# Performance work log

Measured on AMD Instinct MI355X. Metric: run time of the kernel, lower is better.

Reference implementation:

```python
import jax, jax.numpy as jnp
import numpy as np
from jax import lax

B, T_DEC, T_ENC = 32, 400, 300
N_MEL, PRENET, ENC_D = 80, 256, 512
ATT_RNN, DEC_RNN, ATT_D = 512, 512, 128
LOC_F, LOC_K = 32, 31


def setup_inputs() -> dict:
    key = jax.random.key(0)
    ks = jax.random.split(key, 24)

    def w(k, shape):
        return jax.random.normal(k, shape, jnp.float32) / np.float32(np.sqrt(shape[-1]))

    inp = {
        "encoder_out": jax.random.normal(ks[0], (B, T_ENC, ENC_D), jnp.float32),
        "mels": jax.random.normal(ks[1], (B, T_DEC, N_MEL), jnp.float32),
        "lengths": jax.random.randint(ks[2], (B,), 1, T_ENC + 1).astype(jnp.int32),
        # prenet (3 layers, no bias)
        "W_p0": w(ks[3], (PRENET, N_MEL)),
        "W_p1": w(ks[4], (PRENET, PRENET)),
        "W_p2": w(ks[5], (PRENET, PRENET)),
        # attention GRUCell: input = prenet_dim + enc_dim = 768
        "W_ih_a": w(ks[6], (3 * ATT_RNN, PRENET + ENC_D)),
        "W_hh_a": w(ks[7], (3 * ATT_RNN, ATT_RNN)),
        "b_ih_a": jnp.zeros((3 * ATT_RNN,), jnp.float32),
        "b_hh_a": jnp.zeros((3 * ATT_RNN,), jnp.float32),
        # decoder GRUCell: input = attn_rnn + enc_dim = 1024 (what the code actually feeds)
        "W_ih_d": w(ks[8], (3 * DEC_RNN, ATT_RNN + ENC_D)),
        "W_hh_d": w(ks[9], (3 * DEC_RNN, DEC_RNN)),
        "b_ih_d": jnp.zeros((3 * DEC_RNN,), jnp.float32),
        "b_hh_d": jnp.zeros((3 * DEC_RNN,), jnp.float32),
        # location-sensitive attention
        "W_q": w(ks[10], (ATT_D, ATT_RNN)),
        "W_m": w(ks[11], (ATT_D, ENC_D)),
        "K_loc": w(ks[12], (LOC_F, 2, LOC_K)),
        "W_l": w(ks[13], (ATT_D, LOC_F)),
        "v": w(ks[14], (ATT_D,)),
        # output projection + gate
        "W_out": w(ks[15], (N_MEL, DEC_RNN + ENC_D)),
        "b_out": jnp.zeros((N_MEL,), jnp.float32),
        "W_g": w(ks[16], (1, DEC_RNN + ENC_D)),
        "b_g": jnp.zeros((1,), jnp.float32),
    }
    return inp


def _gru_cell(x, h, W_ih, W_hh, b_ih, b_hh):
    gi = x @ W_ih.T + b_ih
    gh = h @ W_hh.T + b_hh
    i_r, i_z, i_n = jnp.split(gi, 3, axis=-1)
    h_r, h_z, h_n = jnp.split(gh, 3, axis=-1)
    r = jax.nn.sigmoid(i_r + h_r)
    z = jax.nn.sigmoid(i_z + h_z)
    n = jnp.tanh(i_n + r * h_n)
    return (1.0 - z) * n + z * h


def _decoder_core(encoder_out, mels, lengths, W_p0, W_p1, W_p2,
                  W_ih_a, W_hh_a, b_ih_a, b_hh_a, W_ih_d, W_hh_d, b_ih_d, b_hh_d,
                  W_q, W_m, K_loc, W_l, v, W_out, b_out, W_g, b_g):
    Bb, T_enc, _ = encoder_out.shape
    T_dec = mels.shape[1]
    pmem = encoder_out @ W_m.T  # [B,T_enc,ATT_D], computed once
    enc_mask = jnp.arange(T_enc)[None, :] < lengths[:, None]  # [B,T_enc]
    # shifted teacher-forcing inputs: zero first frame, then mels[:, :-1]
    dec_inputs = jnp.concatenate(
        [jnp.zeros((Bb, 1, mels.shape[2]), mels.dtype), mels[:, :-1]], axis=1)
    drop_key = jax.random.key(42)
    pad = LOC_K // 2

    def prenet(x, t):
        for i, W in enumerate((W_p0, W_p1, W_p2)):
            x = jax.nn.relu(x @ W.T)
            k = jax.random.fold_in(drop_key, t * 3 + i)
            keep = jax.random.bernoulli(k, 0.5, x.shape)
            x = jnp.where(keep, x * 2.0, 0.0)  # inverted dropout p=0.5 (hardcoded training=True)
        return x

    def step(carry, xs):
        ah, dh, ctx, aw, aw_sum = carry
        frame, t = xs
        x = prenet(frame, t)
        ah = _gru_cell(jnp.concatenate([x, ctx], -1), ah, W_ih_a, W_hh_a, b_ih_a, b_hh_a)
        # location features from current + cumulative attention weights
        awc = jnp.stack([aw, aw_sum], axis=1)  # [B,2,T_enc]
        loc = lax.conv_general_dilated(awc, K_loc, (1,), [(pad, pad)],
                                       dimension_numbers=("NCH", "OIH", "NCH"))
        loc = jnp.swapaxes(loc, 1, 2) @ W_l.T  # [B,T_enc,ATT_D]
        e = jnp.tanh((ah @ W_q.T)[:, None, :] + pmem + loc) @ v  # [B,T_enc]
        e = jnp.where(enc_mask, e, -1e9)
        aw_new = jax.nn.softmax(e, axis=-1)
        ctx = jnp.einsum("bt,btd->bd", aw_new, encoder_out)
        aw_sum = aw_sum + aw_new
        dh = _gru_cell(jnp.concatenate([ah, ctx], -1), dh, W_ih_d, W_hh_d, b_ih_d, b_hh_d)
        dhc = jnp.concatenate([dh, ctx], -1)
        mel = dhc @ W_out.T + b_out  # [B,N_MEL]
        gate = (dhc @ W_g.T + b_g)[:, 0]  # [B]
        return (ah, dh, ctx, aw_new, aw_sum), (mel, gate, aw_new)

    f32 = encoder_out.dtype
    init = (jnp.zeros((Bb, ATT_RNN), f32), jnp.zeros((Bb, DEC_RNN), f32),
            jnp.zeros((Bb, ENC_D), f32), jnp.zeros((Bb, T_enc), f32),
            jnp.zeros((Bb, T_enc), f32))
    frames = jnp.swapaxes(dec_inputs, 0, 1)  # [T_dec,B,N_MEL]
    _, (mels_out, gates, aligns) = lax.scan(jax.checkpoint(step), init,
                                            (frames, jnp.arange(T_dec)))
    mel_outputs = jnp.transpose(mels_out, (1, 2, 0))  # [B,N_MEL,T_dec]
    gate_outputs = jnp.swapaxes(gates, 0, 1)          # [B,T_dec]
    alignments = jnp.swapaxes(aligns, 0, 1)           # [B,T_dec,T_enc]
    return mel_outputs, gate_outputs, alignments


def reference(encoder_out, mels, lengths, W_p0, W_p1, W_p2,
              W_ih_a, W_hh_a, b_ih_a, b_hh_a, W_ih_d, W_hh_d, b_ih_d, b_hh_d,
              W_q, W_m, K_loc, W_l, v, W_out, b_out, W_g, b_g):
    return _decoder_core(encoder_out, mels, lengths, W_p0, W_p1, W_p2,
                         W_ih_a, W_hh_a, b_ih_a, b_hh_a, W_ih_d, W_hh_d, b_ih_d, b_hh_d,
                         W_q, W_m, K_loc, W_l, v, W_out, b_out, W_g, b_g)
```

## Files before the change

### kernel.cpp

```cpp
#include <hip/hip_runtime.h>
#include <cstdint>


static constexpr int TDEC = 400, TENC = 300, NMEL = 80;

__device__ __forceinline__ uint2 threefry2x32(uint32_t k0, uint32_t k1,
                                              uint32_t x0, uint32_t x1) {
  uint32_t k2 = k0 ^ k1 ^ 0x1BD11BDAu;
  x0 += k0; x1 += k1;
#define TFR(r) { x0 += x1; x1 = (x1 << (r)) | (x1 >> (32 - (r))); x1 ^= x0; }
  TFR(13) TFR(15) TFR(26) TFR(6)
  x0 += k1; x1 += k2 + 1u;
  TFR(17) TFR(29) TFR(16) TFR(24)
  x0 += k2; x1 += k0 + 2u;
  TFR(13) TFR(15) TFR(26) TFR(6)
  x0 += k0; x1 += k1 + 3u;
  TFR(17) TFR(29) TFR(16) TFR(24)
  x0 += k1; x1 += k2 + 4u;
  TFR(13) TFR(15) TFR(26) TFR(6)
  x0 += k2; x1 += k0 + 5u;
#undef TFR
  return make_uint2(x0, x1);
}

__device__ __forceinline__ bool keep_mask(uint32_t key0, uint32_t key1, uint32_t idx) {
  uint2 o = threefry2x32(key0, key1, 0u, idx);
  uint32_t bits = o.x ^ o.y;
  float u = __uint_as_float((bits >> 9) | 0x3f800000u) - 1.0f;
  return u < 0.5f;
}

__device__ __forceinline__ float dot4(float4 w, float4 a) {
  return w.x * a.x + w.y * a.y + w.z * a.z + w.w * a.w;
}
__device__ __forceinline__ float nt_load(const float* p) {
  return __builtin_nontemporal_load(p);
}

template <int K>
__device__ __forceinline__ void prenet_layer(const float* in_lds, float* out_lds,
                                             float* out_g, const float* __restrict__ W,
                                             uint32_t key0, uint32_t key1, int b0) {
  const int tid = threadIdx.x;
  const int cgp = tid & 63, bg = tid >> 6;
  float acc[4][4];
#pragma unroll
  for (int cc = 0; cc < 4; ++cc)
#pragma unroll
    for (int rr = 0; rr < 4; ++rr) acc[cc][rr] = 0.f;
  const float4* W4 = (const float4*)W;
  const float4* in4 = (const float4*)in_lds;
  for (int k4 = 0; k4 < K / 4; ++k4) {
    float4 a[4];
#pragma unroll
    for (int rr = 0; rr < 4; ++rr) a[rr] = in4[(bg * 4 + rr) * (K / 4) + k4];
#pragma unroll
    for (int cc = 0; cc < 4; ++cc) {
      float4 w = W4[(cgp + 64 * cc) * (K / 4) + k4];
#pragma unroll
      for (int rr = 0; rr < 4; ++rr) acc[cc][rr] += dot4(w, a[rr]);
    }
  }
#pragma unroll
  for (int cc = 0; cc < 4; ++cc)
#pragma unroll
    for (int rr = 0; rr < 4; ++rr) {
      int c = cgp + 64 * cc, br = bg * 4 + rr;
      float val = fmaxf(acc[cc][rr], 0.f);
      val = keep_mask(key0, key1, (uint32_t)((b0 + br) * 256 + c)) ? val * 2.f : 0.f;
      if (out_lds) out_lds[br * 256 + c] = val;
      if (out_g) out_g[(b0 + br) * 256 + c] = val;
    }
  __syncthreads();
}

__global__ __launch_bounds__(256) void prenet_kernel(const float* __restrict__ mels,
                                                     const float* __restrict__ Wp0,
                                                     const float* __restrict__ Wp1,
                                                     const float* __restrict__ Wp2,
                                                     float* __restrict__ x_all) {
  __shared__ float bufA[16 * 256];
  __shared__ float bufB[16 * 256];
  const int t = blockIdx.x >> 1, b0 = (blockIdx.x & 1) * 16;
  const int tid = threadIdx.x;
  for (int i = tid; i < 16 * 80; i += 256) {
    int br = i / 80, k = i % 80;
    bufB[br * 80 + k] = (t == 0) ? 0.f : mels[((b0 + br) * TDEC + (t - 1)) * NMEL + k];
  }
  __syncthreads();
  uint2 k0v = threefry2x32(0u, 42u, 0u, (uint32_t)(t * 3 + 0));
  uint2 k1v = threefry2x32(0u, 42u, 0u, (uint32_t)(t * 3 + 1));
  uint2 k2v = threefry2x32(0u, 42u, 0u, (uint32_t)(t * 3 + 2));
  prenet_layer<80>(bufB, bufA, nullptr, Wp0, k0v.x, k0v.y, b0);
  prenet_layer<256>(bufA, bufB, nullptr, Wp1, k1v.x, k1v.y, b0);
  prenet_layer<256>(bufB, nullptr, x_all + t * 8192, Wp2, k2v.x, k2v.y, b0);
}

__global__ __launch_bounds__(256) void pmem_kernel(const float* __restrict__ enc,
                                                   const float* __restrict__ Wm,
                                                   float* __restrict__ pmem) {
  const int b = blockIdx.x / 10, pc = blockIdx.x % 10;
  const int j = threadIdx.x & 127, ph = threadIdx.x >> 7;
  const float4* Wm4 = (const float4*)Wm;
  const float4* enc4 = (const float4*)enc + (size_t)(b * 300 + pc * 30 + ph * 15) * 128;
  float acc[15];
#pragma unroll
  for (int pp = 0; pp < 15; ++pp) acc[pp] = 0.f;
  for (int k4 = 0; k4 < 128; ++k4) {
    float4 w = Wm4[j * 128 + k4];
#pragma unroll
    for (int pp = 0; pp < 15; ++pp) acc[pp] += dot4(w, enc4[pp * 128 + k4]);
  }
#pragma unroll
  for (int pp = 0; pp < 15; ++pp)
    pmem[(size_t)(b * 300 + pc * 30 + ph * 15 + pp) * 128 + j] = acc[pp];
}

struct GP {
  const float *xall, *enc, *pmem;
  const int* lens;
  const float *Wiha, *Whha, *biha, *bhha;
  const float *Wihd, *Whhd, *bihd, *bhhd;
  const float *Wq, *Kloc, *Wl, *vv, *Wout, *bout, *Wg, *bg;
  float *ah, *dh;
  float *e2;
  float *pM, *pS;
  float *V;
  float *awsum2;
  float *omel, *ogate, *oalign;
};

template <int KIN>
__device__ __forceinline__ void gru_phase(const float4* __restrict__ A4, int a4n,
                                          const float4* B4,
                                          const float4* __restrict__ H4,
                                          const float* __restrict__ Wih,
                                          const float* __restrict__ Whh,
                                          const float* __restrict__ bih,
                                          const float* __restrict__ bhh,
                                          const float* __restrict__ hprev,
                                          float* __restrict__ hout,
                                          int idx0, float* lds) {
  const int tid = threadIdx.x;
  const int row = tid >> 3, seg = tid & 7;
  constexpr int K4I = KIN / 4;
  constexpr int SI = K4I / 8;
  const float4* Wih4 = (const float4*)Wih;
  const float4* Whh4 = (const float4*)Whh;
  float acc[24];
#pragma unroll
  for (int g = 0; g < 24; ++g) acc[g] = 0.f;
  for (int s = 0; s < SI; ++s) {
    int k4 = seg * SI + s;
    float4 a = (k4 < a4n) ? A4[row * a4n + k4] : B4[row * 128 + (k4 - a4n)];
#pragma unroll
    for (int gate = 0; gate < 3; ++gate)
#pragma unroll
      for (int i = 0; i < 4; ++i)
        acc[gate * 4 + i] += dot4(Wih4[(size_t)(gate * 512 + idx0 + i) * K4I + k4], a);
  }
  for (int s = 0; s < 16; ++s) {
    int k4 = seg * 16 + s;
    float4 a = H4[row * 128 + k4];
#pragma unroll
    for (int gate = 0; gate < 3; ++gate)
#pragma unroll
      for (int i = 0; i < 4; ++i)
        acc[12 + gate * 4 + i] += dot4(Whh4[(size_t)(gate * 512 + idx0 + i) * 128 + k4], a);
  }
#pragma unroll
  for (int g = 0; g < 24; ++g) lds[(g * 32 + row) * 8 + seg] = acc[g];
  __syncthreads();
  if (tid < 128) {
    int i = tid >> 5, r = tid & 31;
    float gi[3], gh[3];
#pragma unroll
    for (int gate = 0; gate < 3; ++gate) {
      float si = 0.f, sh = 0.f;
#pragma unroll
      for (int s = 0; s < 8; ++s) {
        si += lds[((gate * 4 + i) * 32 + r) * 8 + s];
        sh += lds[((12 + gate * 4 + i) * 32 + r) * 8 + s];
      }
      gi[gate] = si + bih[gate * 512 + idx0 + i];
      gh[gate] = sh + bhh[gate * 512 + idx0 + i];
    }
    float rr = 1.f / (1.f + expf(-(gi[0] + gh[0])));
    float zz = 1.f / (1.f + expf(-(gi[1] + gh[1])));
    float nn = tanhf(gi[2] + rr * gh[2]);
    float hp = hprev[r * 512 + idx0 + i];
    hout[r * 512 + idx0 + i] = (1.f - zz) * nn + zz * hp;
  }
}

__global__ __launch_bounds__(256) void k_gru(GP P, int t) {
  __shared__ float lds[6144];
  __shared__ float ctxS[16384];
  __shared__ float wqL[128];
  const int tid = threadIdx.x, blk = blockIdx.x;
  const int p0 = t & 1, p1 = p0 ^ 1;

  if (t == 0) {
    for (int i = tid; i < 16384; i += 256) ctxS[i] = 0.f;
  } else {
    if (tid < 128) {
      int row = tid >> 2, q = tid & 3;
      float m = -3.4e38f;
#pragma unroll
      for (int j = 0; j < 4; ++j) m = fmaxf(m, P.pM[p1 * 128 + row * 4 + j]);
      float z = 0.f;
#pragma unroll
      for (int j = 0; j < 4; ++j)
        z += P.pS[p1 * 128 + row * 4 + j] * expf(P.pM[p1 * 128 + row * 4 + j] - m);
      wqL[tid] = expf(P.pM[p1 * 128 + row * 4 + q] - m) / z;
    }
    __syncthreads();
    const float* Vb = P.V + (size_t)p1 * 65536;
    for (int i = tid; i < 16384; i += 256) {
      int row = i >> 9, c = i & 511;
      const float* v = Vb + (size_t)(row * 4) * 512 + c;
      ctxS[i] = v[0] * wqL[row * 4 + 0] + v[512] * wqL[row * 4 + 1] +
                v[1024] * wqL[row * 4 + 2] + v[1536] * wqL[row * 4 + 3];
    }
  }
  __syncthreads();

  if (blk < 128) {
    if (t < TDEC)
      gru_phase<768>((const float4*)(P.xall + (size_t)t * 8192), 64,
                     (const float4*)ctxS,
                     (const float4*)(P.ah + p1 * 16384),
                     P.Wiha, P.Whha, P.biha, P.bhha,
                     P.ah + p1 * 16384, P.ah + p0 * 16384, blk * 4, lds);
  } else {
    if (t >= 1)
      gru_phase<1024>((const float4*)(P.ah + p1 * 16384), 128,
                      (const float4*)ctxS,
                      (const float4*)(P.dh + p0 * 16384),
                      P.Wihd, P.Whhd, P.bihd, P.bhhd,
                      P.dh + p0 * 16384, P.dh + p1 * 16384, (blk - 128) * 4, lds);
  }
}

__global__ __launch_bounds__(256) void k_energy(GP P, int t) {
  __shared__ float smem[5400];
  const int tid = threadIdx.x, blk = blockIdx.x;
  const int p0 = t & 1, p1 = p0 ^ 1;

  if (blk >= 128) {
    if (t < 1) return;
    const int r = blk - 128;
    float* dhcx = smem;
    float* opl = smem + 1024;
    float M = -3.4e38f;
#pragma unroll
    for (int j = 0; j < 4; ++j) M = fmaxf(M, P.pM[p1 * 128 + r * 4 + j]);
    float Z = 0.f;
#pragma unroll
    for (int j = 0; j < 4; ++j)
      Z += P.pS[p1 * 128 + r * 4 + j] * expf(P.pM[p1 * 128 + r * 4 + j] - M);
    float w0 = expf(P.pM[p1 * 128 + r * 4 + 0] - M) / Z;
    float w1 = expf(P.pM[p1 * 128 + r * 4 + 1] - M) / Z;
    float w2 = expf(P.pM[p1 * 128 + r * 4 + 2] - M) / Z;
    float w3 = expf(P.pM[p1 * 128 + r * 4 + 3] - M) / Z;
    const float* Vb = P.V + (size_t)p1 * 65536 + (size_t)(r * 4) * 512;
    for (int i = tid; i < 512; i += 256) {
      dhcx[i] = P.dh[p1 * 16384 + r * 512 + i];
      dhcx[512 + i] = Vb[i] * w0 + Vb[512 + i] * w1 + Vb[1024 + i] * w2 + Vb[1536 + i] * w3;
    }
    __syncthreads();
    if (tid < 162) {
      int m = tid >> 1, h = tid & 1;
      const float4* W4 = (m < 80) ? ((const float4*)P.Wout + (size_t)m * 256)
                                  : (const float4*)P.Wg;
      const float4* x4 = (const float4*)dhcx;
      float a = 0.f;
      for (int k4 = h * 128; k4 < h * 128 + 128; ++k4) a += dot4(W4[k4], x4[k4]);
      opl[tid] = a;
    }
    __syncthreads();
    if (tid < 81) {
      float sum = opl[tid * 2] + opl[tid * 2 + 1];
      if (tid < 80) P.omel[(size_t)(r * 80 + tid) * 400 + (t - 1)] = sum + P.bout[tid];
      else P.ogate[r * 400 + (t - 1)] = sum + P.bg[0];
    }
    return;
  }

  const int r = blk >> 2, q = blk & 3;
  const int pb = q * 75;
  float* awW = smem;
  float* asW = smem + 108;
  float2* t2f = (float2*)(smem + 216);
  float* convl = smem + 2200;
  float* qpL = smem + 4632;
  float* qbL = smem + 4888;
  float* el = smem + 5016;
  float* eex = smem + 5096;

  if (t >= 1) {
    float M = -3.4e38f;
#pragma unroll
    for (int j = 0; j < 4; ++j) M = fmaxf(M, P.pM[p1 * 128 + r * 4 + j]);
    float Z = 0.f;
#pragma unroll
    for (int j = 0; j < 4; ++j)
      Z += P.pS[p1 * 128 + r * 4 + j] * expf(P.pM[p1 * 128 + r * 4 + j] - M);
    float inv = 1.f / Z;
    for (int i = tid; i < 105; i += 256) {
      int p = pb - 15 + i;
      float a = 0.f, s = 0.f;
      if (p >= 0 && p < TENC) {
        a = expf(P.e2[p1 * 9728 + r * 304 + p] - M) * inv;
        s = P.awsum2[p1 * 9600 + r * 300 + p] + a;
      }
      awW[i] = a;
      asW[i] = s;
      if (p >= pb && p < pb + 75) {
        P.awsum2[p0 * 9600 + r * 300 + p] = s;
        P.oalign[((size_t)(r * 400 + (t - 1))) * 300 + p] = a;
      }
    }
  } else {
    for (int i = tid; i < 105; i += 256) { awW[i] = 0.f; asW[i] = 0.f; }
  }
  if (t >= TDEC) return;

  for (int i = tid; i < 992; i += 256) {
    int f = i / 31, k = i % 31;
    t2f[i] = make_float2(P.Kloc[f * 62 + k], P.Kloc[f * 62 + 31 + k]);
  }
  __syncthreads();

  {
    int f = tid & 31, pl0 = tid >> 5;
    for (int pl = pl0; pl < 75; pl += 8) {
      float a = 0.f;
#pragma unroll
      for (int k = 0; k < 31; ++k) {
        float2 tv = t2f[f * 31 + k];
        a += awW[pl + k] * tv.x + asW[pl + k] * tv.y;
      }
      convl[f * 76 + pl] = a;
    }
  }
  {
    int j = tid & 127, kh = tid >> 7;
    const float4* Wq4 = (const float4*)P.Wq;
    const float4* a4 = (const float4*)(P.ah + p0 * 16384 + r * 512);
    float acc = 0.f;
    for (int k4 = kh * 64; k4 < kh * 64 + 64; ++k4) acc += dot4(Wq4[j * 128 + k4], a4[k4]);
    qpL[j * 2 + kh] = acc;
  }
  __syncthreads();
  if (tid < 128) qbL[tid] = qpL[tid * 2] + qpL[tid * 2 + 1];
  __syncthreads();
  {
    int w = tid >> 6, lane = tid & 63;
    float wl0[32], wl1[32];
#pragma unroll
    for (int f = 0; f < 32; ++f) {
      wl0[f] = P.Wl[lane * 32 + f];
      wl1[f] = P.Wl[(lane + 64) * 32 + f];
    }
    float v0 = P.vv[lane], v1 = P.vv[lane + 64];
    float q0 = qbL[lane], q1 = qbL[64 + lane];
    int len = P.lens[r];
    for (int pl = w; pl < 75; pl += 4) {
      int p = pb + pl;
      float a0 = 0.f, a1 = 0.f;
#pragma unroll
      for (int f = 0; f < 32; ++f) {
        float c = convl[f * 76 + pl];
        a0 += c * wl0[f];
        a1 += c * wl1[f];
      }
      float e0 = tanhf(q0 + P.pmem[((size_t)r * 300 + p) * 128 + lane] + a0) * v0;
      float e1 = tanhf(q1 + P.pmem[((size_t)r * 300 + p) * 128 + 64 + lane] + a1) * v1;
      float es = e0 + e1;
#pragma unroll
      for (int off = 32; off > 0; off >>= 1) es += __shfl_xor(es, off, 64);
      if (lane == 0) {
        float ev = (p < len) ? es : -1e9f;
        P.e2[p0 * 9728 + r * 304 + p] = ev;
        el[pl] = ev;
      }
    }
  }
  __syncthreads();
  if (tid < 64) {
    int lane = tid;
    float m = -3.4e38f;
    for (int i = lane; i < 75; i += 64) m = fmaxf(m, el[i]);
#pragma unroll
    for (int off = 32; off > 0; off >>= 1) m = fmaxf(m, __shfl_xor(m, off, 64));
    float s = 0.f;
    for (int i = lane; i < 75; i += 64) {
      float x = expf(el[i] - m);
      eex[i] = x;
      s += x;
    }
#pragma unroll
    for (int off = 32; off > 0; off >>= 1) s += __shfl_xor(s, off, 64);
    if (lane == 0) {
      P.pM[p0 * 128 + r * 4 + q] = m;
      P.pS[p0 * 128 + r * 4 + q] = s;
    }
  }
  __syncthreads();
  {
    float* Vw = P.V + (size_t)p0 * 65536 + (size_t)(r * 4 + q) * 512;
#pragma unroll
    for (int cc = 0; cc < 2; ++cc) {
      int c = tid + cc * 256;
      float acc = 0.f;
      const float* eb = P.enc + ((size_t)(r * 300 + pb)) * 512 + c;
      for (int po = 0; po < 75; ++po) acc += eex[po] * nt_load(eb + (size_t)po * 512);
      Vw[c] = acc;
    }
  }
}

extern "C" void kernel_launch(void* const* d_in, const int* in_sizes, int n_in,
                              void* d_out, int out_size, void* d_ws, size_t ws_size,
                              hipStream_t stream) {
  const float* enc = (const float*)d_in[0];
  const float* mels = (const float*)d_in[1];
  const int* lens = (const int*)d_in[2];
  const float* Wp0 = (const float*)d_in[3];
  const float* Wp1 = (const float*)d_in[4];
  const float* Wp2 = (const float*)d_in[5];

  float* ws = (float*)d_ws;
  float* x_all = ws;
  float* pmem = x_all + 3276800;
  float* ah = pmem + 1228800;
  float* dh = ah + 32768;
  float* e2 = dh + 32768;
  float* pM = e2 + 19456;
  float* pS = pM + 256;
  float* V = pS + 256;
  float* awsum2 = V + 131072;

  (void)hipMemsetAsync(ah, 0, (32768 + 32768) * sizeof(float), stream);
  (void)hipMemsetAsync(awsum2, 0, 19200 * sizeof(float), stream);

  prenet_kernel<<<800, 256, 0, stream>>>(mels, Wp0, Wp1, Wp2, x_all);
  pmem_kernel<<<320, 256, 0, stream>>>(enc, (const float*)d_in[15], pmem);

  float* omel = (float*)d_out;
  float* ogate = omel + 32 * 80 * 400;
  float* oalign = ogate + 32 * 400;

  GP P;
  P.xall = x_all; P.enc = enc; P.pmem = pmem; P.lens = lens;
  P.Wiha = (const float*)d_in[6]; P.Whha = (const float*)d_in[7];
  P.biha = (const float*)d_in[8]; P.bhha = (const float*)d_in[9];
  P.Wihd = (const float*)d_in[10]; P.Whhd = (const float*)d_in[11];
  P.bihd = (const float*)d_in[12]; P.bhhd = (const float*)d_in[13];
  P.Wq = (const float*)d_in[14]; P.Kloc = (const float*)d_in[16];
  P.Wl = (const float*)d_in[17]; P.vv = (const float*)d_in[18];
  P.Wout = (const float*)d_in[19]; P.bout = (const float*)d_in[20];
  P.Wg = (const float*)d_in[21]; P.bg = (const float*)d_in[22];
  P.ah = ah; P.dh = dh; P.e2 = e2; P.pM = pM; P.pS = pS; P.V = V;
  P.awsum2 = awsum2;
  P.omel = omel; P.ogate = ogate; P.oalign = oalign;

  for (int t = 0; t <= TDEC; ++t) {
    k_gru<<<256, 256, 0, stream>>>(P, t);
    k_energy<<<160, 256, 0, stream>>>(P, t);
  }
}
```

Baseline: 50.05 ms.

## Fuse decoder timestep loop into one persistent kernel with grid barriers

Replaces the 802 per-timestep kernel launches with a single persistent 256-block kernel. Blocks synchronise through hand-written atomic grid barriers, and each block keeps its GRU weight slice pinned in LDS for all steps. The attention context is now reduced once per row by a leader block and written to a ctxM buffer, instead of being recomputed by every GRU block. This removes launch overhead and repeated weight reloads, but relies on all 256 blocks being co-resident, since otherwise the spin barriers deadlock, and adds atomic-load overhead on shared state.

```diff
diff --git a/kernel.cpp b/kernel.cpp
--- a/kernel.cpp
+++ b/kernel.cpp
@@ -37,6 +37,45 @@
   return __builtin_nontemporal_load(p);
 }
 
+__device__ __forceinline__ void s_rel(float* p, float v) {
+  __hip_atomic_store(p, v, __ATOMIC_RELAXED, __HIP_MEMORY_SCOPE_AGENT);
+}
+__device__ __forceinline__ float l_rel(const float* p) {
+  return __hip_atomic_load(p, __ATOMIC_RELAXED, __HIP_MEMORY_SCOPE_AGENT);
+}
+__device__ __forceinline__ float4 l4(const float4* p) {
+  const unsigned long long* q = (const unsigned long long*)p;
+  unsigned long long a = __hip_atomic_load(q, __ATOMIC_RELAXED, __HIP_MEMORY_SCOPE_AGENT);
+  unsigned long long b = __hip_atomic_load(q + 1, __ATOMIC_RELAXED, __HIP_MEMORY_SCOPE_AGENT);
+  float4 r;
+  ((unsigned long long*)&r)[0] = a;
+  ((unsigned long long*)&r)[1] = b;
+  return r;
+}
+
+__device__ __forceinline__ void gsync(int* arrive, int* release, int bno) {
+  __syncthreads();
+  if (blockIdx.x == 0) {
+    if (threadIdx.x > 0)
+      while (__hip_atomic_load(&arrive[threadIdx.x * 32], __ATOMIC_RELAXED,
+                               __HIP_MEMORY_SCOPE_AGENT) < bno)
+        __builtin_amdgcn_s_sleep(16);
+    __syncthreads();
+    if (threadIdx.x < 8)
+      __hip_atomic_store(&release[threadIdx.x * 32], bno, __ATOMIC_RELEASE,
+                         __HIP_MEMORY_SCOPE_AGENT);
+  } else {
+    if (threadIdx.x == 0) {
+      __hip_atomic_store(&arrive[blockIdx.x * 32], bno, __ATOMIC_RELEASE,
+                         __HIP_MEMORY_SCOPE_AGENT);
+      while (__hip_atomic_load(&release[(blockIdx.x & 7) * 32], __ATOMIC_RELAXED,
+                               __HIP_MEMORY_SCOPE_AGENT) < bno)
+        __builtin_amdgcn_s_sleep(16);
+    }
+  }
+  __syncthreads();
+}
+
 template <int K>
 __device__ __forceinline__ void prenet_layer(const float* in_lds, float* out_lds,
                                              float* out_g, const float* __restrict__ W,
@@ -116,308 +155,319 @@
     pmem[(size_t)(b * 300 + pc * 30 + ph * 15 + pp) * 128 + j] = acc[pp];
 }
 
-struct GP {
+struct DP {
   const float *xall, *enc, *pmem;
   const int* lens;
   const float *Wiha, *Whha, *biha, *bhha;
   const float *Wihd, *Whhd, *bihd, *bhhd;
   const float *Wq, *Kloc, *Wl, *vv, *Wout, *bout, *Wg, *bg;
-  float *ah, *dh;
+  float *ah, *dh, *ctxM;
   float *e2;
   float *pM, *pS;
   float *V;
   float *awsum2;
+  int *arrive, *release, *rM;
   float *omel, *ogate, *oalign;
 };
 
-template <int KIN>
-__device__ __forceinline__ void gru_phase(const float4* __restrict__ A4, int a4n,
-                                          const float4* B4,
-                                          const float4* __restrict__ H4,
-                                          const float* __restrict__ Wih,
-                                          const float* __restrict__ Whh,
-                                          const float* __restrict__ bih,
-                                          const float* __restrict__ bhh,
-                                          const float* __restrict__ hprev,
-                                          float* __restrict__ hout,
-                                          int idx0, float* lds) {
-  const int tid = threadIdx.x;
-  const int row = tid >> 3, seg = tid & 7;
-  constexpr int K4I = KIN / 4;
-  constexpr int SI = K4I / 8;
-  const float4* Wih4 = (const float4*)Wih;
-  const float4* Whh4 = (const float4*)Whh;
-  float acc[24];
-#pragma unroll
-  for (int g = 0; g < 24; ++g) acc[g] = 0.f;
-  for (int s = 0; s < SI; ++s) {
-    int k4 = seg * SI + s;
-    float4 a = (k4 < a4n) ? A4[row * a4n + k4] : B4[row * 128 + (k4 - a4n)];
-#pragma unroll
-    for (int gate = 0; gate < 3; ++gate)
-#pragma unroll
-      for (int i = 0; i < 4; ++i)
-        acc[gate * 4 + i] += dot4(Wih4[(size_t)(gate * 512 + idx0 + i) * K4I + k4], a);
-  }
-  for (int s = 0; s < 16; ++s) {
-    int k4 = seg * 16 + s;
-    float4 a = H4[row * 128 + k4];
-#pragma unroll
-    for (int gate = 0; gate < 3; ++gate)
-#pragma unroll
-      for (int i = 0; i < 4; ++i)
-        acc[12 + gate * 4 + i] += dot4(Whh4[(size_t)(gate * 512 + idx0 + i) * 128 + k4], a);
-  }
-#pragma unroll
-  for (int g = 0; g < 24; ++g) lds[(g * 32 + row) * 8 + seg] = acc[g];
-  __syncthreads();
-  if (tid < 128) {
-    int i = tid >> 5, r = tid & 31;
-    float gi[3], gh[3];
-#pragma unroll
-    for (int gate = 0; gate < 3; ++gate) {
-      float si = 0.f, sh = 0.f;
-#pragma unroll
-      for (int s = 0; s < 8; ++s) {
-        si += lds[((gate * 4 + i) * 32 + r) * 8 + s];
-        sh += lds[((12 + gate * 4 + i) * 32 + r) * 8 + s];
-      }
-      gi[gate] = si + bih[gate * 512 + idx0 + i];
-      gh[gate] = sh + bhh[gate * 512 + idx0 + i];
-    }
-    float rr = 1.f / (1.f + expf(-(gi[0] + gh[0])));
-    float zz = 1.f / (1.f + expf(-(gi[1] + gh[1])));
-    float nn = tanhf(gi[2] + rr * gh[2]);
-    float hp = hprev[r * 512 + idx0 + i];
-    hout[r * 512 + idx0 + i] = (1.f - zz) * nn + zz * hp;
-  }
-}
-
-__global__ __launch_bounds__(256) void k_gru(GP P, int t) {
-  __shared__ float lds[6144];
-  __shared__ float ctxS[16384];
-  __shared__ float wqL[128];
+__global__ __launch_bounds__(256, 1) void decoder_kernel(DP P) {
+  __shared__ float4 pinW[4608];
+  __shared__ float scr[6144];
+  __shared__ float2 tapsL[992];
   const int tid = threadIdx.x, blk = blockIdx.x;
-  const int p0 = t & 1, p1 = p0 ^ 1;
-
-  if (t == 0) {
-    for (int i = tid; i < 16384; i += 256) ctxS[i] = 0.f;
+  const int er = blk >> 2, eq = blk & 3, pb = eq * 75;
+
+  if (blk < 128) {
+    const float4* Wih4 = (const float4*)P.Wiha;
+    const float4* Whh4 = (const float4*)P.Whha;
+    int idx0 = blk * 4;
+    for (int i = tid; i < 2304; i += 256) {
+      int g = i / 768, rem = i % 768, r2 = rem / 192, k4 = rem % 192;
+      pinW[i] = Wih4[(size_t)(g * 512 + idx0 + r2) * 192 + k4];
+    }
+    for (int i = tid; i < 1536; i += 256) {
+      int g = i / 512, rem = i % 512, r2 = rem / 128, k4 = rem % 128;
+      pinW[2304 + i] = Whh4[(size_t)(g * 512 + idx0 + r2) * 128 + k4];
+    }
   } else {
-    if (tid < 128) {
-      int row = tid >> 2, q = tid & 3;
-      float m = -3.4e38f;
-#pragma unroll
-      for (int j = 0; j < 4; ++j) m = fmaxf(m, P.pM[p1 * 128 + row * 4 + j]);
-      float z = 0.f;
-#pragma unroll
-      for (int j = 0; j < 4; ++j)
-        z += P.pS[p1 * 128 + row * 4 + j] * expf(P.pM[p1 * 128 + row * 4 + j] - m);
-      wqL[tid] = expf(P.pM[p1 * 128 + row * 4 + q] - m) / z;
-    }
-    __syncthreads();
-    const float* Vb = P.V + (size_t)p1 * 65536;
-    for (int i = tid; i < 16384; i += 256) {
-      int row = i >> 9, c = i & 511;
-      const float* v = Vb + (size_t)(row * 4) * 512 + c;
-      ctxS[i] = v[0] * wqL[row * 4 + 0] + v[512] * wqL[row * 4 + 1] +
-                v[1024] * wqL[row * 4 + 2] + v[1536] * wqL[row * 4 + 3];
-    }
-  }
-  __syncthreads();
-
-  if (blk < 128) {
-    if (t < TDEC)
-      gru_phase<768>((const float4*)(P.xall + (size_t)t * 8192), 64,
-                     (const float4*)ctxS,
-                     (const float4*)(P.ah + p1 * 16384),
-                     P.Wiha, P.Whha, P.biha, P.bhha,
-                     P.ah + p1 * 16384, P.ah + p0 * 16384, blk * 4, lds);
-  } else {
-    if (t >= 1)
-      gru_phase<1024>((const float4*)(P.ah + p1 * 16384), 128,
-                      (const float4*)ctxS,
-                      (const float4*)(P.dh + p0 * 16384),
-                      P.Wihd, P.Whhd, P.bihd, P.bhhd,
-                      P.dh + p0 * 16384, P.dh + p1 * 16384, (blk - 128) * 4, lds);
-  }
-}
-
-__global__ __launch_bounds__(256) void k_energy(GP P, int t) {
-  __shared__ float smem[5400];
-  const int tid = threadIdx.x, blk = blockIdx.x;
-  const int p0 = t & 1, p1 = p0 ^ 1;
-
-  if (blk >= 128) {
-    if (t < 1) return;
-    const int r = blk - 128;
-    float* dhcx = smem;
-    float* opl = smem + 1024;
-    float M = -3.4e38f;
-#pragma unroll
-    for (int j = 0; j < 4; ++j) M = fmaxf(M, P.pM[p1 * 128 + r * 4 + j]);
-    float Z = 0.f;
-#pragma unroll
-    for (int j = 0; j < 4; ++j)
-      Z += P.pS[p1 * 128 + r * 4 + j] * expf(P.pM[p1 * 128 + r * 4 + j] - M);
-    float w0 = expf(P.pM[p1 * 128 + r * 4 + 0] - M) / Z;
-    float w1 = expf(P.pM[p1 * 128 + r * 4 + 1] - M) / Z;
-    float w2 = expf(P.pM[p1 * 128 + r * 4 + 2] - M) / Z;
-    float w3 = expf(P.pM[p1 * 128 + r * 4 + 3] - M) / Z;
-    const float* Vb = P.V + (size_t)p1 * 65536 + (size_t)(r * 4) * 512;
-    for (int i = tid; i < 512; i += 256) {
-      dhcx[i] = P.dh[p1 * 16384 + r * 512 + i];
-      dhcx[512 + i] = Vb[i] * w0 + Vb[512 + i] * w1 + Vb[1024 + i] * w2 + Vb[1536 + i] * w3;
-    }
-    __syncthreads();
-    if (tid < 162) {
-      int m = tid >> 1, h = tid & 1;
-      const float4* W4 = (m < 80) ? ((const float4*)P.Wout + (size_t)m * 256)
-                                  : (const float4*)P.Wg;
-      const float4* x4 = (const float4*)dhcx;
-      float a = 0.f;
-      for (int k4 = h * 128; k4 < h * 128 + 128; ++k4) a += dot4(W4[k4], x4[k4]);
-      opl[tid] = a;
-    }
-    __syncthreads();
-    if (tid < 81) {
-      float sum = opl[tid * 2] + opl[tid * 2 + 1];
-      if (tid < 80) P.omel[(size_t)(r * 80 + tid) * 400 + (t - 1)] = sum + P.bout[tid];
-      else P.ogate[r * 400 + (t - 1)] = sum + P.bg[0];
-    }
-    return;
-  }
-
-  const int r = blk >> 2, q = blk & 3;
-  const int pb = q * 75;
-  float* awW = smem;
-  float* asW = smem + 108;
-  float2* t2f = (float2*)(smem + 216);
-  float* convl = smem + 2200;
-  float* qpL = smem + 4632;
-  float* qbL = smem + 4888;
-  float* el = smem + 5016;
-  float* eex = smem + 5096;
-
-  if (t >= 1) {
-    float M = -3.4e38f;
-#pragma unroll
-    for (int j = 0; j < 4; ++j) M = fmaxf(M, P.pM[p1 * 128 + r * 4 + j]);
-    float Z = 0.f;
-#pragma unroll
-    for (int j = 0; j < 4; ++j)
-      Z += P.pS[p1 * 128 + r * 4 + j] * expf(P.pM[p1 * 128 + r * 4 + j] - M);
-    float inv = 1.f / Z;
-    for (int i = tid; i < 105; i += 256) {
-      int p = pb - 15 + i;
-      float a = 0.f, s = 0.f;
-      if (p >= 0 && p < TENC) {
-        a = expf(P.e2[p1 * 9728 + r * 304 + p] - M) * inv;
-        s = P.awsum2[p1 * 9600 + r * 300 + p] + a;
-      }
-      awW[i] = a;
-      asW[i] = s;
-      if (p >= pb && p < pb + 75) {
-        P.awsum2[p0 * 9600 + r * 300 + p] = s;
-        P.oalign[((size_t)(r * 400 + (t - 1))) * 300 + p] = a;
-      }
-    }
-  } else {
-    for (int i = tid; i < 105; i += 256) { awW[i] = 0.f; asW[i] = 0.f; }
-  }
-  if (t >= TDEC) return;
-
+    const float4* Wih4 = (const float4*)P.Wihd;
+    const float4* Whh4 = (const float4*)P.Whhd;
+    int idx0 = (blk - 128) * 4;
+    for (int i = tid; i < 3072; i += 256) {
+      int g = i / 1024, rem = i % 1024, r2 = rem / 256, k4 = rem % 256;
+      pinW[i] = Wih4[(size_t)(g * 512 + idx0 + r2) * 256 + k4];
+    }
+    for (int i = tid; i < 1536; i += 256) {
+      int g = i / 512, rem = i % 512, r2 = rem / 128, k4 = rem % 128;
+      pinW[3072 + i] = Whh4[(size_t)(g * 512 + idx0 + r2) * 128 + k4];
+    }
+  }
   for (int i = tid; i < 992; i += 256) {
     int f = i / 31, k = i % 31;
-    t2f[i] = make_float2(P.Kloc[f * 62 + k], P.Kloc[f * 62 + 31 + k]);
+    tapsL[i] = make_float2(P.Kloc[f * 62 + k], P.Kloc[f * 62 + 31 + k]);
   }
   __syncthreads();
 
-  {
-    int f = tid & 31, pl0 = tid >> 5;
-    for (int pl = pl0; pl < 75; pl += 8) {
-      float a = 0.f;
-#pragma unroll
-      for (int k = 0; k < 31; ++k) {
-        float2 tv = t2f[f * 31 + k];
-        a += awW[pl + k] * tv.x + asW[pl + k] * tv.y;
+  int bno = 0;
+  for (int t = 0; t <= TDEC; ++t) {
+    const int p0 = t & 1, p1 = p0 ^ 1;
+
+    {
+      const bool isAtt = (blk < 128);
+      const bool act = isAtt ? (t < TDEC) : (t >= 1);
+      if (act) {
+        const int row = tid >> 3, seg = tid & 7;
+        const int idx0 = (isAtt ? blk : (blk - 128)) * 4;
+        const int K4I = isAtt ? 192 : 256;
+        const int SI = K4I / 8, a4n = isAtt ? 64 : 128;
+        const float4* WihL = pinW;
+        const float4* WhhL = pinW + (isAtt ? 2304 : 3072);
+        const float4* A4p = isAtt ? (const float4*)(P.xall + (size_t)t * 8192) : nullptr;
+        const float4* Ab = isAtt ? nullptr : (const float4*)(P.ah + p1 * 16384);
+        const float4* C4 = (const float4*)(P.ctxM + p1 * 16384);
+        const float4* H4 = isAtt ? (const float4*)(P.ah + p1 * 16384)
+                                 : (const float4*)(P.dh + p0 * 16384);
+        const float* bih = isAtt ? P.biha : P.bihd;
+        const float* bhh = isAtt ? P.bhha : P.bhhd;
+        const float* hpv = isAtt ? (P.ah + p1 * 16384) : (P.dh + p0 * 16384);
+        float* hout = isAtt ? (P.ah + p0 * 16384) : (P.dh + p1 * 16384);
+
+        float acc[24];
+#pragma unroll
+        for (int g = 0; g < 24; ++g) acc[g] = 0.f;
+        for (int s = 0; s < SI; ++s) {
+          int k4 = seg * SI + s;
+          float4 a;
+          if (k4 < a4n) a = isAtt ? A4p[row * a4n + k4] : l4(&Ab[row * a4n + k4]);
+          else a = l4(&C4[row * 128 + (k4 - a4n)]);
+#pragma unroll
+          for (int g = 0; g < 3; ++g)
+#pragma unroll
+            for (int i = 0; i < 4; ++i)
+              acc[g * 4 + i] += dot4(WihL[(g * 4 + i) * K4I + k4], a);
+        }
+        for (int s = 0; s < 16; ++s) {
+          int k4 = seg * 16 + s;
+          float4 h = l4(&H4[row * 128 + k4]);
+#pragma unroll
+          for (int g = 0; g < 3; ++g)
+#pragma unroll
+            for (int i = 0; i < 4; ++i)
+              acc[12 + g * 4 + i] += dot4(WhhL[(g * 4 + i) * 128 + k4], h);
+        }
+#pragma unroll
+        for (int g = 0; g < 24; ++g) scr[(g * 32 + row) * 8 + seg] = acc[g];
+        __syncthreads();
+        if (tid < 128) {
+          int i = tid >> 5, r = tid & 31;
+          float gi[3], gh[3];
+#pragma unroll
+          for (int g = 0; g < 3; ++g) {
+            float si = 0.f, sh = 0.f;
+#pragma unroll
+            for (int s = 0; s < 8; ++s) {
+              si += scr[((g * 4 + i) * 32 + r) * 8 + s];
+              sh += scr[((12 + g * 4 + i) * 32 + r) * 8 + s];
+            }
+            gi[g] = si + bih[g * 512 + idx0 + i];
+            gh[g] = sh + bhh[g * 512 + idx0 + i];
+          }
+          float rr = 1.f / (1.f + expf(-(gi[0] + gh[0])));
+          float zz = 1.f / (1.f + expf(-(gi[1] + gh[1])));
+          float nn = tanhf(gi[2] + rr * gh[2]);
+          float hp = l_rel(&hpv[r * 512 + idx0 + i]);
+          s_rel(&hout[r * 512 + idx0 + i], (1.f - zz) * nn + zz * hp);
+        }
       }
-      convl[f * 76 + pl] = a;
-    }
-  }
-  {
-    int j = tid & 127, kh = tid >> 7;
-    const float4* Wq4 = (const float4*)P.Wq;
-    const float4* a4 = (const float4*)(P.ah + p0 * 16384 + r * 512);
-    float acc = 0.f;
-    for (int k4 = kh * 64; k4 < kh * 64 + 64; ++k4) acc += dot4(Wq4[j * 128 + k4], a4[k4]);
-    qpL[j * 2 + kh] = acc;
-  }
-  __syncthreads();
-  if (tid < 128) qbL[tid] = qpL[tid * 2] + qpL[tid * 2 + 1];
-  __syncthreads();
-  {
-    int w = tid >> 6, lane = tid & 63;
-    float wl0[32], wl1[32];
-#pragma unroll
-    for (int f = 0; f < 32; ++f) {
-      wl0[f] = P.Wl[lane * 32 + f];
-      wl1[f] = P.Wl[(lane + 64) * 32 + f];
-    }
-    float v0 = P.vv[lane], v1 = P.vv[lane + 64];
-    float q0 = qbL[lane], q1 = qbL[64 + lane];
-    int len = P.lens[r];
-    for (int pl = w; pl < 75; pl += 4) {
-      int p = pb + pl;
-      float a0 = 0.f, a1 = 0.f;
-#pragma unroll
-      for (int f = 0; f < 32; ++f) {
-        float c = convl[f * 76 + pl];
-        a0 += c * wl0[f];
-        a1 += c * wl1[f];
+    }
+    gsync(P.arrive, P.release, ++bno);
+
+    if (blk < 128) {
+      float* awW = scr;
+      float* asW = scr + 105;
+      float* convl = scr + 216;
+      float* qp = scr + 2656;
+      float* qb = scr + 2912;
+      float* el = scr + 3040;
+      float* eex = scr + 3120;
+
+      if (t >= 1) {
+        float M = -3.4e38f;
+#pragma unroll
+        for (int j = 0; j < 4; ++j) M = fmaxf(M, l_rel(&P.pM[p1 * 128 + er * 4 + j]));
+        float Z = 0.f;
+#pragma unroll
+        for (int j = 0; j < 4; ++j)
+          Z += l_rel(&P.pS[p1 * 128 + er * 4 + j]) *
+               expf(l_rel(&P.pM[p1 * 128 + er * 4 + j]) - M);
+        float inv = 1.f / Z;
+        for (int i = tid; i < 105; i += 256) {
+          int p = pb - 15 + i;
+          float a = 0.f, s = 0.f;
+          if (p >= 0 && p < TENC) {
+            a = expf(l_rel(&P.e2[p1 * 9728 + er * 304 + p]) - M) * inv;
+            s = l_rel(&P.awsum2[p1 * 9600 + er * 300 + p]) + a;
+          }
+          awW[i] = a;
+          asW[i] = s;
+          if (p >= pb && p < pb + 75) {
+            s_rel(&P.awsum2[p0 * 9600 + er * 300 + p], s);
+            P.oalign[((size_t)(er * 400 + (t - 1))) * 300 + p] = a;
+          }
+        }
+      } else {
+        for (int i = tid; i < 105; i += 256) { awW[i] = 0.f; asW[i] = 0.f; }
       }
-      float e0 = tanhf(q0 + P.pmem[((size_t)r * 300 + p) * 128 + lane] + a0) * v0;
-      float e1 = tanhf(q1 + P.pmem[((size_t)r * 300 + p) * 128 + 64 + lane] + a1) * v1;
-      float es = e0 + e1;
-#pragma unroll
-      for (int off = 32; off > 0; off >>= 1) es += __shfl_xor(es, off, 64);
-      if (lane == 0) {
-        float ev = (p < len) ? es : -1e9f;
-        P.e2[p0 * 9728 + r * 304 + p] = ev;
-        el[pl] = ev;
+      __syncthreads();
+
+      if (t < TDEC) {
+        {
+          int f = tid & 31, pl0 = tid >> 5;
+          for (int pl = pl0; pl < 75; pl += 8) {
+            float a = 0.f;
+#pragma unroll
+            for (int k = 0; k < 31; ++k) {
+              float2 tv = tapsL[f * 31 + k];
+              a += awW[pl + k] * tv.x + asW[pl + k] * tv.y;
+            }
+            convl[f * 76 + pl] = a;
+          }
+        }
+        {
+          int j = tid & 127, kh = tid >> 7;
+          const float4* Wq4 = (const float4*)P.Wq;
+          const float4* a4 = (const float4*)(P.ah + p0 * 16384 + er * 512);
+          float acc = 0.f;
+          for (int k4 = kh * 64; k4 < kh * 64 + 64; ++k4)
+            acc += dot4(Wq4[j * 128 + k4], l4(&a4[k4]));
+          qp[j * 2 + kh] = acc;
+        }
+        __syncthreads();
+        if (tid < 128) qb[tid] = qp[tid * 2] + qp[tid * 2 + 1];
+        __syncthreads();
+        {
+          int w = tid >> 6, lane = tid & 63;
+          float wl0[32], wl1[32];
+#pragma unroll
+          for (int f = 0; f < 32; ++f) {
+            wl0[f] = P.Wl[lane * 32 + f];
+            wl1[f] = P.Wl[(lane + 64) * 32 + f];
+          }
+          float v0 = P.vv[lane], v1 = P.vv[lane + 64];
+          float q0 = qb[lane], q1 = qb[64 + lane];
+          int len = P.lens[er];
+          for (int pl = w; pl < 75; pl += 4) {
+            int p = pb + pl;
+            float a0 = 0.f, a1 = 0.f;
+#pragma unroll
+            for (int f = 0; f < 32; ++f) {
+              float c = convl[f * 76 + pl];
+              a0 += c * wl0[f];
+              a1 += c * wl1[f];
+            }
+            float e0 = tanhf(q0 + P.pmem[((size_t)er * 300 + p) * 128 + lane] + a0) * v0;
+            float e1 = tanhf(q1 + P.pmem[((size_t)er * 300 + p) * 128 + 64 + lane] + a1) * v1;
+            float es = e0 + e1;
+#pragma unroll
+            for (int off = 32; off > 0; off >>= 1) es += __shfl_xor(es, off, 64);
+            if (lane == 0) {
+              float ev = (p < len) ? es : -1e9f;
+              s_rel(&P.e2[p0 * 9728 + er * 304 + p], ev);
+              el[pl] = ev;
+            }
+          }
+        }
+        __syncthreads();
+        if (tid < 64) {
+          int lane = tid;
+          float m = -3.4e38f;
+          for (int i = lane; i < 75; i += 64) m = fmaxf(m, el[i]);
+#pragma unroll
+          for (int off = 32; off > 0; off >>= 1) m = fmaxf(m, __shfl_xor(m, off, 64));
+          float s = 0.f;
+          for (int i = lane; i < 75; i += 64) {
+            float x = expf(el[i] - m);
+            eex[i] = x;
+            s += x;
+          }
+#pragma unroll
+          for (int off = 32; off > 0; off >>= 1) s += __shfl_xor(s, off, 64);
+          if (lane == 0) {
+            s_rel(&P.pM[p0 * 128 + er * 4 + eq], m);
+            s_rel(&P.pS[p0 * 128 + er * 4 + eq], s);
+          }
+        }
+        __syncthreads();
+        {
+          float* Vw = P.V + (size_t)p0 * 65536 + (size_t)(er * 4 + eq) * 512;
+#pragma unroll
+          for (int cc = 0; cc < 2; ++cc) {
+            int c = tid + cc * 256;
+            float acc = 0.f;
+            const float* eb = P.enc + ((size_t)(er * 300 + pb)) * 512 + c;
+            for (int po = 0; po < 75; ++po) acc += eex[po] * nt_load(eb + (size_t)po * 512);
+            s_rel(&Vw[c], acc);
+          }
+        }
+        __syncthreads();
+        if (tid == 0)
+          __hip_atomic_store(&P.rM[(er * 4 + eq) * 32], t + 1, __ATOMIC_RELEASE,
+                             __HIP_MEMORY_SCOPE_AGENT);
+        if (eq == 0) {
+          if (tid < 3)
+            while (__hip_atomic_load(&P.rM[(er * 4 + 1 + tid) * 32], __ATOMIC_RELAXED,
+                                     __HIP_MEMORY_SCOPE_AGENT) < t + 1)
+              __builtin_amdgcn_s_sleep(8);
+          __syncthreads();
+          float M = -3.4e38f;
+#pragma unroll
+          for (int j = 0; j < 4; ++j) M = fmaxf(M, l_rel(&P.pM[p0 * 128 + er * 4 + j]));
+          float Z = 0.f, wq[4];
+#pragma unroll
+          for (int j = 0; j < 4; ++j) {
+            wq[j] = expf(l_rel(&P.pM[p0 * 128 + er * 4 + j]) - M);
+            Z += l_rel(&P.pS[p0 * 128 + er * 4 + j]) * wq[j];
+          }
+          float invZ = 1.f / Z;
+          const float* Vb = P.V + (size_t)p0 * 65536 + (size_t)(er * 4) * 512;
+#pragma unroll
+          for (int cc = 0; cc < 2; ++cc) {
+            int c = tid + cc * 256;
+            float acc = 0.f;
+#pragma unroll
+            for (int j = 0; j < 4; ++j) acc += l_rel(&Vb[j * 512 + c]) * wq[j];
+            s_rel(&P.ctxM[p0 * 16384 + er * 512 + c], acc * invZ);
+          }
+        }
       }
-    }
-  }
-  __syncthreads();
-  if (tid < 64) {
-    int lane = tid;
-    float m = -3.4e38f;
-    for (int i = lane; i < 75; i += 64) m = fmaxf(m, el[i]);
-#pragma unroll
-    for (int off = 32; off > 0; off >>= 1) m = fmaxf(m, __shfl_xor(m, off, 64));
-    float s = 0.f;
-    for (int i = lane; i < 75; i += 64) {
-      float x = expf(el[i] - m);
-      eex[i] = x;
-      s += x;
-    }
-#pragma unroll
-    for (int off = 32; off > 0; off >>= 1) s += __shfl_xor(s, off, 64);
-    if (lane == 0) {
-      P.pM[p0 * 128 + r * 4 + q] = m;
-      P.pS[p0 * 128 + r * 4 + q] = s;
-    }
-  }
-  __syncthreads();
-  {
-    float* Vw = P.V + (size_t)p0 * 65536 + (size_t)(r * 4 + q) * 512;
-#pragma unroll
-    for (int cc = 0; cc < 2; ++cc) {
-      int c = tid + cc * 256;
-      float acc = 0.f;
-      const float* eb = P.enc + ((size_t)(r * 300 + pb)) * 512 + c;
-      for (int po = 0; po < 75; ++po) acc += eex[po] * nt_load(eb + (size_t)po * 512);
-      Vw[c] = acc;
-    }
+    } else if (blk < 160) {
+      if (t >= 1) {
+        const int r = blk - 128;
+        float* dhcx = scr;
+        float* opl = scr + 1024;
+        for (int i = tid; i < 512; i += 256) {
+          dhcx[i] = l_rel(&P.dh[p1 * 16384 + r * 512 + i]);
+          dhcx[512 + i] = l_rel(&P.ctxM[p1 * 16384 + r * 512 + i]);
+        }
+        __syncthreads();
+        if (tid < 162) {
+          int m = tid >> 1, h = tid & 1;
+          const float4* W4 = (m < 80) ? ((const float4*)P.Wout + (size_t)m * 256)
+                                      : (const float4*)P.Wg;
+          const float4* x4 = (const float4*)dhcx;
+          float a = 0.f;
+          for (int k4 = h * 128; k4 < h * 128 + 128; ++k4) a += dot4(W4[k4], x4[k4]);
+          opl[tid] = a;
+        }
+        __syncthreads();
+        if (tid < 81) {
+          float sum = opl[tid * 2] + opl[tid * 2 + 1];
+          if (tid < 80) P.omel[(size_t)(r * 80 + tid) * 400 + (t - 1)] = sum + P.bout[tid];
+          else P.ogate[r * 400 + (t - 1)] = sum + P.bg[0];
+        }
+      }
+    }
+    gsync(P.arrive, P.release, ++bno);
   }
 }
 
@@ -427,32 +477,36 @@
   const float* enc = (const float*)d_in[0];
   const float* mels = (const float*)d_in[1];
   const int* lens = (const int*)d_in[2];
-  const float* Wp0 = (const float*)d_in[3];
-  const float* Wp1 = (const float*)d_in[4];
-  const float* Wp2 = (const float*)d_in[5];
 
   float* ws = (float*)d_ws;
   float* x_all = ws;
   float* pmem = x_all + 3276800;
   float* ah = pmem + 1228800;
   float* dh = ah + 32768;
-  float* e2 = dh + 32768;
+  float* ctxM = dh + 32768;
+  float* e2 = ctxM + 32768;
   float* pM = e2 + 19456;
   float* pS = pM + 256;
   float* V = pS + 256;
   float* awsum2 = V + 131072;
-
-  (void)hipMemsetAsync(ah, 0, (32768 + 32768) * sizeof(float), stream);
+  int* arrive = (int*)(awsum2 + 19200);
+  int* release = arrive + 8192;
+  int* rM = release + 256;
+
+  (void)hipMemsetAsync(ah, 0, (3 * 32768) * sizeof(float), stream);
   (void)hipMemsetAsync(awsum2, 0, 19200 * sizeof(float), stream);
-
-  prenet_kernel<<<800, 256, 0, stream>>>(mels, Wp0, Wp1, Wp2, x_all);
+  (void)hipMemsetAsync(arrive, 0, (8192 + 256 + 4096) * sizeof(int), stream);
+
+  prenet_kernel<<<800, 256, 0, stream>>>(mels, (const float*)d_in[3],
+                                         (const float*)d_in[4], (const float*)d_in[5],
+                                         x_all);
   pmem_kernel<<<320, 256, 0, stream>>>(enc, (const float*)d_in[15], pmem);
 
   float* omel = (float*)d_out;
   float* ogate = omel + 32 * 80 * 400;
   float* oalign = ogate + 32 * 400;
 
-  GP P;
+  DP P;
   P.xall = x_all; P.enc = enc; P.pmem = pmem; P.lens = lens;
   P.Wiha = (const float*)d_in[6]; P.Whha = (const float*)d_in[7];
   P.biha = (const float*)d_in[8]; P.bhha = (const float*)d_in[9];
@@ -462,12 +516,10 @@
   P.Wl = (const float*)d_in[17]; P.vv = (const float*)d_in[18];
   P.Wout = (const float*)d_in[19]; P.bout = (const float*)d_in[20];
   P.Wg = (const float*)d_in[21]; P.bg = (const float*)d_in[22];
-  P.ah = ah; P.dh = dh; P.e2 = e2; P.pM = pM; P.pS = pS; P.V = V;
+  P.ah = ah; P.dh = dh; P.ctxM = ctxM; P.e2 = e2; P.pM = pM; P.pS = pS; P.V = V;
   P.awsum2 = awsum2;
+  P.arrive = arrive; P.release = release; P.rM = rM;
   P.omel = omel; P.ogate = ogate; P.oalign = oalign;
 
-  for (int t = 0; t <= TDEC; ++t) {
-    k_gru<<<256, 256, 0, stream>>>(P, t);
-    k_energy<<<160, 256, 0, stream>>>(P, t);
-  }
-}
+  decoder_kernel<<<256, 256, 0, stream>>>(P);
+}
```

Measured after the change: 57.81 ms. +15.5%, slower.
